# Kernel tuning notes

Hardware: AMD Instinct MI355X
Metric: run time of the kernel (lower is better)

## Reference

```python
import jax, jax.numpy as jnp
import numpy as np

B, S, D = 2, 2048, 2048
HQ, HK, HD = 16, 8, 128          # query heads, kv heads, head_dim
EPS = 1e-6
ROPE_THETA = 10000.0
SCALE = HD ** -0.5


def setup_inputs() -> dict:
    key = jax.random.key(0)
    ks = jax.random.split(key, 6)
    s = lambda fan_in: 1.0 / np.sqrt(fan_in)
    return {
        "hidden_states": jax.random.normal(ks[0], (B, S, D), jnp.float32),
        "positions": jnp.arange(S, dtype=jnp.int32),
        "Wq": jax.random.normal(ks[1], (D, HQ * HD), jnp.float32) * s(D),
        "Wk": jax.random.normal(ks[2], (D, HK * HD), jnp.float32) * s(D),
        "Wv": jax.random.normal(ks[3], (D, HK * HD), jnp.float32) * s(D),
        "Wo": jax.random.normal(ks[4], (HQ * HD, D), jnp.float32) * s(HQ * HD),
        "q_norm_w": jnp.ones((HD,), jnp.float32),
        "k_norm_w": jnp.ones((HD,), jnp.float32),
    }


def _rmsnorm(x, w):
    # RMSNorm over last (head_dim) axis, as in q_norm/k_norm
    var = jnp.mean(jnp.square(x), axis=-1, keepdims=True)
    return x * jax.lax.rsqrt(var + EPS) * w


def _rope(x, positions):
    # x: [B, S, H, HD]; rotate_half-style RoPE (Qwen3 convention)
    half = HD // 2
    inv_freq = 1.0 / (ROPE_THETA ** (jnp.arange(0, half, dtype=jnp.float32) / half))
    angles = positions.astype(jnp.float32)[:, None] * inv_freq[None, :]  # [S, half]
    cos = jnp.cos(angles)[None, :, None, :]  # [1, S, 1, half]
    sin = jnp.sin(angles)[None, :, None, :]
    x1, x2 = x[..., :half], x[..., half:]
    return jnp.concatenate([x1 * cos - x2 * sin, x2 * cos + x1 * sin], axis=-1)


def reference(hidden_states, positions, Wq, Wk, Wv, Wo, q_norm_w, k_norm_w):
    b, s, _ = hidden_states.shape
    q = (hidden_states @ Wq).reshape(b, s, HQ, HD)
    k = (hidden_states @ Wk).reshape(b, s, HK, HD)
    v = (hidden_states @ Wv).reshape(b, s, HK, HD)

    q = _rmsnorm(q, q_norm_w)
    k = _rmsnorm(k, k_norm_w)

    q = _rope(q, positions)
    k = _rope(k, positions)

    # GQA: repeat KV heads to match query heads
    groups = HQ // HK
    k = jnp.repeat(k, groups, axis=2)  # [B, S, HQ, HD]
    v = jnp.repeat(v, groups, axis=2)

    scores = jnp.einsum("bqhd,bkhd->bhqk", q, k) * SCALE  # [B, HQ, S, S]
    causal = jnp.tril(jnp.ones((s, s), dtype=bool))
    scores = jnp.where(causal[None, None], scores, jnp.float32(-jnp.inf))
    attn = jax.nn.softmax(scores, axis=-1)

    out = jnp.einsum("bhqk,bkhd->bqhd", attn, v).reshape(b, s, HQ * HD)
    return out @ Wo
```

## Files before the change

### kernel.cpp

```cpp
#include <hip/hip_runtime.h>
#include <cstdint>
#include <cstddef>

typedef _Float16 half8 __attribute__((ext_vector_type(8)));
typedef _Float16 half4 __attribute__((ext_vector_type(4)));
typedef float f32x4 __attribute__((ext_vector_type(4)));

#define DI __device__ __forceinline__

DI void gld_lds16(void* sp, const void* gp) {
  __builtin_amdgcn_global_load_lds(
      (const __attribute__((address_space(1))) void*)gp,
      (__attribute__((address_space(3))) void*)sp, 16, 0, 0);
}

template <int N>
DI void vmwait() { asm volatile("s_waitcnt vmcnt(%0)" :: "n"(N) : "memory"); }

DI void barrier_raw() {
  asm volatile("" ::: "memory");
  __builtin_amdgcn_s_barrier();
  asm volatile("" ::: "memory");
}

DI unsigned pk16(float a, float b) {
  _Float16 ha = (_Float16)a, hb = (_Float16)b;
  unsigned short ua = __builtin_bit_cast(unsigned short, ha);
  unsigned short ub = __builtin_bit_cast(unsigned short, hb);
  return (unsigned)ua | ((unsigned)ub << 16);
}

__global__ __launch_bounds__(256) void prep(const float* __restrict__ hs,
                                            const float* __restrict__ Wq,
                                            const float* __restrict__ Wk,
                                            const float* __restrict__ Wv,
                                            const float* __restrict__ Wo,
                                            _Float16* __restrict__ Xh,
                                            _Float16* __restrict__ Wqkvt,
                                            _Float16* __restrict__ Wot) {
  const int bid = blockIdx.x;
  if (bid >= 12288) {
    const int i = (bid - 12288) * 256 + threadIdx.x;
    const float4* p = (const float4*)hs + (size_t)i * 2;
    const float4 a = p[0], b = p[1];
    half8 h;
    h[0] = (_Float16)a.x; h[1] = (_Float16)a.y; h[2] = (_Float16)a.z; h[3] = (_Float16)a.w;
    h[4] = (_Float16)b.x; h[5] = (_Float16)b.y; h[6] = (_Float16)b.z; h[7] = (_Float16)b.w;
    *(half8*)(Xh + (size_t)i * 8) = h;
    return;
  }
  const float* in;
  _Float16* outp;
  int C, t;
  if (bid < 4096)      { in = Wq; outp = Wqkvt;                        C = 2048; t = bid; }
  else if (bid < 6144) { in = Wk; outp = Wqkvt + (size_t)2048 * 2048;  C = 1024; t = bid - 4096; }
  else if (bid < 8192) { in = Wv; outp = Wqkvt + (size_t)3072 * 2048;  C = 1024; t = bid - 6144; }
  else                 { in = Wo; outp = Wot;                          C = 2048; t = bid - 8192; }
  __shared__ float tl[32][33];
  const int tx = threadIdx.x & 31, ty = threadIdx.x >> 5;
  const int ctiles = C >> 5;
  const int tc = t % ctiles, tr = t / ctiles;
  const int r0 = tr * 32, c0 = tc * 32;
#pragma unroll
  for (int i = 0; i < 4; i++)
    tl[ty + 8 * i][tx] = in[(size_t)(r0 + ty + 8 * i) * C + c0 + tx];
  __syncthreads();
#pragma unroll
  for (int i = 0; i < 4; i++) {
    const int rr = ty + 8 * i;
    outp[(size_t)(c0 + rr) * 2048 + r0 + tx] = (_Float16)tl[tx][rr];
  }
}

#define QPHASE(Q, STAGE, VMW)                                                  \
  {                                                                            \
    half8 afr[2][2];                                                           \
    _Pragma("unroll") for (int j = 0; j < 2; j++)                              \
      _Pragma("unroll") for (int ks = 0; ks < 2; ks++) {                       \
        const int arow = wm * 128 + ((Q) * 2 + j) * 16 + lo;                   \
        afr[j][ks] =                                                           \
            *(const half8*)&sA[sa][arow * 64 + (((ks * 4 + hi) ^ lo7) << 3)];  \
      }                                                                        \
    STAGE;                                                                     \
    VMW;                                                                       \
    barrier_raw();                                                             \
    asm volatile("s_waitcnt lgkmcnt(0)" ::: "memory");                         \
    __builtin_amdgcn_sched_barrier(0);                                         \
    __builtin_amdgcn_s_setprio(1);                                             \
    _Pragma("unroll") for (int j = 0; j < 2; j++)                              \
      _Pragma("unroll") for (int nf = 0; nf < 4; nf++)                         \
        _Pragma("unroll") for (int ks = 0; ks < 2; ks++)                       \
          acc[(Q) * 2 + j][nf] = __builtin_amdgcn_mfma_f32_16x16x32_f16(       \
              afr[j][ks], bfr[nf][ks], acc[(Q) * 2 + j][nf], 0, 0, 0);         \
    __builtin_amdgcn_s_setprio(0);                                             \
    barrier_raw();                                                             \
  }

__global__ __launch_bounds__(512, 2) void gemm256(const _Float16* __restrict__ A,
                                                  const _Float16* __restrict__ Bt,
                                                  _Float16* __restrict__ C,
                                                  int M, int N, int K) {
  __shared__ _Float16 sA[3][16384];
  __shared__ _Float16 sB[2][16384];
  const int tid = threadIdx.x, w = tid >> 6, l = tid & 63, lo = l & 15, hi = l >> 4;
  const int lo7 = lo & 7;
  const int wm = w >> 2, wn = w & 3;
  const int nbn = N >> 8;
  const int nwg = gridDim.x;
  int bid = blockIdx.x;
  bid = (bid & 7) * (nwg >> 3) + (bid >> 3);
  const int bm0 = (bid / nbn) << 8, bn0 = (bid % nbn) << 8;
  const int cswz = ((tid & 7) ^ ((tid >> 3) & 7)) << 3;
  const int NT = K >> 6;

  auto stageA = [&](int kt, int slot, int i0) {
#pragma unroll
    for (int ii = 0; ii < 2; ++ii) {
      const int i = i0 + ii;
      gld_lds16(&sA[slot][i * 4096 + (w << 9)],
                A + (size_t)(bm0 + i * 64 + (tid >> 3)) * K + kt * 64 + cswz);
    }
  };
  auto stageB = [&](int kt, int slot, int i0) {
#pragma unroll
    for (int ii = 0; ii < 2; ++ii) {
      const int i = i0 + ii;
      gld_lds16(&sB[slot][i * 4096 + (w << 9)],
                Bt + (size_t)(bn0 + i * 64 + (tid >> 3)) * K + kt * 64 + cswz);
    }
  };

  f32x4 acc[8][4];
#pragma unroll
  for (int mf = 0; mf < 8; mf++)
#pragma unroll
    for (int nf = 0; nf < 4; nf++)
#pragma unroll
      for (int r = 0; r < 4; r++) acc[mf][nf][r] = 0.0f;

  stageA(0, 0, 0); stageA(0, 0, 2);
  stageA(1, 1, 0); stageA(1, 1, 2);
  stageB(0, 0, 0); stageB(0, 0, 2);
  vmwait<0>();
  barrier_raw();

  int sa = 0, sa2 = 2;
#pragma unroll 1
  for (int t = 0; t < NT; ++t) {
    const int sb = t & 1, sb1 = sb ^ 1;
    half8 bfr[4][2];
#pragma unroll
    for (int nf = 0; nf < 4; nf++)
#pragma unroll
      for (int ks = 0; ks < 2; ks++) {
        const int brow = wn * 64 + nf * 16 + lo;
        bfr[nf][ks] = *(const half8*)&sB[sb][brow * 64 + (((ks * 4 + hi) ^ lo7) << 3)];
      }
    QPHASE(0, if (t + 1 < NT) stageB(t + 1, sb1, 0), )
    QPHASE(1, if (t + 1 < NT) stageB(t + 1, sb1, 2), )
    QPHASE(2, if (t + 2 < NT) stageA(t + 2, sa2, 0), )
    QPHASE(3, if (t + 2 < NT) stageA(t + 2, sa2, 2),
           if (t + 2 < NT) { vmwait<4>(); } else { vmwait<0>(); })
    sa = (sa == 2) ? 0 : sa + 1;
    sa2 = (sa2 == 2) ? 0 : sa2 + 1;
  }

  const int nfsel = lo >> 2;
  const int sbase = hi * 16 + 4 * (lo & 3);
#pragma unroll
  for (int mf = 0; mf < 8; mf++)
#pragma unroll
    for (int r = 0; r < 4; r++) {
      const unsigned p01 = pk16(acc[mf][0][r], acc[mf][1][r]);
      const unsigned p23 = pk16(acc[mf][2][r], acc[mf][3][r]);
      unsigned h[4];
#pragma unroll
      for (int j = 0; j < 4; j++) {
        const unsigned w01 = (unsigned)__shfl((int)p01, sbase + j, 64);
        const unsigned w23 = (unsigned)__shfl((int)p23, sbase + j, 64);
        const unsigned wp = (nfsel & 2) ? w23 : w01;
        h[j] = (nfsel & 1) ? (wp >> 16) : (wp & 0xffffu);
      }
      const uint2 ov = make_uint2(h[0] | (h[1] << 16), h[2] | (h[3] << 16));
      *(uint2*)&C[(size_t)(bm0 + wm * 128 + mf * 16 + hi * 4 + r) * N +
                  (bn0 + wn * 64 + 4 * lo)] = ov;
    }
}

template <int BM, bool F16OUT>
__global__ __launch_bounds__(256) void gemm_bt(const _Float16* __restrict__ A,
                                               const _Float16* __restrict__ Bt,
                                               void* __restrict__ Cv,
                                               int M, int N, int K) {
  constexpr int MF = BM / 32;
  constexpr int LA = BM / 64;
  __shared__ _Float16 sA[2][BM * 32];
  __shared__ _Float16 sB[2][128 * 32];
  const int tid = threadIdx.x;
  const int w = tid >> 6, l = tid & 63, lo = l & 15, hi = l >> 4;
  const int gx = gridDim.x, nwg = gx * gridDim.y;
  int bid = blockIdx.y * gx + blockIdx.x;
  bid = (bid & 7) * (nwg >> 3) + (bid >> 3);
  const int bn0 = (bid % gx) * 128, bm0 = (bid / gx) * BM;
  const int wm = w >> 1, wn = w & 1;
  const int srow = l >> 2;
  const int csel = ((l & 3) ^ ((l >> 3) & 3)) * 8;
  const int kswz = (hi ^ ((lo >> 1) & 3)) * 8;

  f32x4 acc[MF][4];
#pragma unroll
  for (int mi = 0; mi < MF; mi++)
#pragma unroll
    for (int ni = 0; ni < 4; ni++)
#pragma unroll
      for (int r = 0; r < 4; r++) acc[mi][ni][r] = 0.0f;

  auto stage = [&](int bi, int kt) {
#pragma unroll
    for (int i = 0; i < LA; ++i) {
      const int j = LA * w + i;
      gld_lds16(&sA[bi][j * 512],
                A + (size_t)(bm0 + j * 16 + srow) * K + (size_t)kt * 32 + csel);
    }
#pragma unroll
    for (int i = 0; i < 2; ++i) {
      const int j = 2 * w + i;
      gld_lds16(&sB[bi][j * 512],
                Bt + (size_t)(bn0 + j * 16 + srow) * K + (size_t)kt * 32 + csel);
    }
  };

  stage(0, 0);
  __syncthreads();
  const int KT = K >> 5;
#pragma unroll 1
  for (int kt = 0; kt < KT; ++kt) {
    const int cur = kt & 1;
    if (kt + 1 < KT) stage(cur ^ 1, kt + 1);
    half8 a[MF], b[4];
#pragma unroll
    for (int mi = 0; mi < MF; mi++)
      a[mi] = *(const half8*)&sA[cur][(wm * (BM / 2) + mi * 16 + lo) * 32 + kswz];
#pragma unroll
    for (int ni = 0; ni < 4; ni++)
      b[ni] = *(const half8*)&sB[cur][(wn * 64 + ni * 16 + lo) * 32 + kswz];
#pragma unroll
    for (int mi = 0; mi < MF; mi++)
#pragma unroll
      for (int ni = 0; ni < 4; ni++)
        acc[mi][ni] = __builtin_amdgcn_mfma_f32_16x16x32_f16(a[mi], b[ni], acc[mi][ni], 0, 0, 0);
    __syncthreads();
  }

#pragma unroll
  for (int mi = 0; mi < MF; mi++)
#pragma unroll
    for (int ni = 0; ni < 4; ni++)
#pragma unroll
      for (int r = 0; r < 4; r++) {
        const size_t idx = (size_t)(bm0 + wm * (BM / 2) + mi * 16 + hi * 4 + r) * N +
                           (bn0 + wn * 64 + ni * 16 + lo);
        if constexpr (F16OUT) ((_Float16*)Cv)[idx] = (_Float16)acc[mi][ni][r];
        else                  ((float*)Cv)[idx] = acc[mi][ni][r];
      }
}

__global__ __launch_bounds__(256) void post(const _Float16* __restrict__ QKV,
                                            const int* __restrict__ pos,
                                            const float* __restrict__ qw,
                                            const float* __restrict__ kw,
                                            _Float16* __restrict__ Qb,
                                            _Float16* __restrict__ Kb,
                                            _Float16* __restrict__ Vt) {
  if (blockIdx.x >= 24576) {
    __shared__ _Float16 tt[32][34];
    const int g = blockIdx.x - 24576;
    const int tx = threadIdx.x & 31, ty = threadIdx.x >> 5;
    const int dt = g & 3;
    const int st = (g >> 2) & 63;
    const int bh = g >> 8;
    const _Float16* src = QKV + (size_t)((bh >> 3) * 2048 + st * 32) * 4096 +
                          3072 + (bh & 7) * 128 + dt * 32;
#pragma unroll
    for (int i = 0; i < 4; i++)
      tt[ty + 8 * i][tx] = src[(size_t)(ty + 8 * i) * 4096 + tx];
    __syncthreads();
    _Float16* dst = Vt + ((size_t)bh * 128 + dt * 32) * 2048 + st * 32;
#pragma unroll
    for (int i = 0; i < 4; i++) {
      const int rr = ty + 8 * i;
      dst[(size_t)rr * 2048 + tx] = tt[tx][rr];
    }
    return;
  }
  const int w = threadIdx.x >> 6, l = threadIdx.x & 63;
  const int wv = blockIdx.x * 4 + w;
  const int t = wv / 24, hh = wv - t * 24;
  const int b = t >> 11, s = t & 2047;
  const bool isq = hh < 16;
  const int col = isq ? hh * 128 : 2048 + (hh - 16) * 128;
  const _Float16* x = QKV + (size_t)t * 4096 + col;
  const float x1 = (float)x[l], x2 = (float)x[l + 64];
  float ss = x1 * x1 + x2 * x2;
  ss += __shfl_xor(ss, 32); ss += __shfl_xor(ss, 16); ss += __shfl_xor(ss, 8);
  ss += __shfl_xor(ss, 4);  ss += __shfl_xor(ss, 2);  ss += __shfl_xor(ss, 1);
  const float rn = rsqrtf(ss * 0.0078125f + 1e-6f);
  const float* wt = isq ? qw : kw;
  const float n1 = x1 * rn * wt[l], n2 = x2 * rn * wt[l + 64];
  const float ang = (float)pos[s] * exp2f((float)l * -0.2076205059304601f);
  float sa, ca;
  sincosf(ang, &sa, &ca);
  const float qs = isq ? 0.12751731f : 1.0f;
  const float o1 = (n1 * ca - n2 * sa) * qs;
  const float o2 = (n2 * ca + n1 * sa) * qs;
  _Float16* dst = isq ? Qb + (((size_t)b * 16 + hh) * 2048 + s) * 128
                      : Kb + (((size_t)b * 8 + (hh - 16)) * 2048 + s) * 128;
  dst[l] = (_Float16)o1;
  dst[l + 64] = (_Float16)o2;
}

__global__ __launch_bounds__(256) void attn_fwd(const _Float16* __restrict__ Q,
                                                const _Float16* __restrict__ K,
                                                const _Float16* __restrict__ Vt,
                                                _Float16* __restrict__ AO) {
  __shared__ _Float16 sK[2][64 * 128];
  __shared__ _Float16 sV[2][128 * 64];
  __shared__ _Float16 P[4][16 * 72];
  const int tid = threadIdx.x, w = tid >> 6, l = tid & 63, lo = l & 15, hi = l >> 4;
  const int qt = 31 - (blockIdx.x >> 5);
  const int hq = blockIdx.x & 15;
  const int b = (blockIdx.x >> 4) & 1;
  const int hk = hq >> 1, q0 = qt * 64;
  const _Float16* Qh = Q + ((size_t)(b * 16 + hq) * 2048) * 128;
  const _Float16* Kh = K + ((size_t)(b * 8 + hk) * 2048) * 128;
  const _Float16* Vh = Vt + ((size_t)(b * 8 + hk) * 128) * 2048;
  const int qw0 = q0 + w * 16;

  auto stageK = [&](int bi, int kv0) {
#pragma unroll
    for (int i = 0; i < 4; ++i) {
      const int inst = w * 4 + i;
      const int r = inst * 4 + (l >> 4);
      const int cb = ((l & 15) * 16) ^ ((r & 7) << 4);
      gld_lds16(&sK[bi][inst * 512],
                (const char*)Kh + (size_t)(kv0 + r) * 256 + cb);
    }
  };
  auto stageV = [&](int bi, int kv0) {
#pragma unroll
    for (int i = 0; i < 4; ++i) {
      const int inst = w * 4 + i;
      const int r = inst * 8 + (l >> 3);
      const int cb = ((l & 7) * 16) ^ ((r & 7) << 4);
      gld_lds16(&sV[bi][inst * 512],
                (const char*)Vh + (size_t)r * 4096 + (size_t)kv0 * 2 + cb);
    }
  };

  half8 aq[4];
#pragma unroll
  for (int kc = 0; kc < 4; kc++)
    aq[kc] = *(const half8*)(Qh + (size_t)(qw0 + lo) * 128 + kc * 32 + hi * 8);

  f32x4 o[8];
#pragma unroll
  for (int dn = 0; dn < 8; dn++)
#pragma unroll
    for (int r = 0; r < 4; r++) o[dn][r] = 0.0f;
  float mrow = -1e30f, lrow = 0.0f;

  const int nt = qt + 1;
  stageK(0, 0);
  stageV(0, 0);
  __syncthreads();
#pragma unroll 1
  for (int kt = 0; kt < nt; ++kt) {
    const int kv0 = kt * 64;
    const int cur = kt & 1;
    if (kt + 1 < nt) {
      stageK(cur ^ 1, kv0 + 64);
      stageV(cur ^ 1, kv0 + 64);
    }
    const char* kb = (const char*)sK[cur];
    const char* vb = (const char*)sV[cur];
    f32x4 s[4];
#pragma unroll
    for (int ns = 0; ns < 4; ns++) {
#pragma unroll
      for (int r = 0; r < 4; r++) s[ns][r] = 0.0f;
      const int krow = ns * 16 + lo;
#pragma unroll
      for (int kc = 0; kc < 4; kc++) {
        half8 bk = *(const half8*)(kb + krow * 256 +
                                   ((kc * 64 + hi * 16) ^ ((krow & 7) << 4)));
        s[ns] = __builtin_amdgcn_mfma_f32_16x16x32_f16(bk, aq[kc], s[ns], 0, 0, 0);
      }
    }
    if (kt == nt - 1) {
#pragma unroll
      for (int ns = 0; ns < 4; ns++) {
        const int kv = kv0 + ns * 16 + hi * 4;
#pragma unroll
        for (int r = 0; r < 4; r++)
          if (kv + r > qw0 + lo) s[ns][r] = -1e30f;
      }
    }
    float tmax = s[0][0];
#pragma unroll
    for (int ns = 0; ns < 4; ns++)
#pragma unroll
      for (int r = 0; r < 4; r++) tmax = fmaxf(tmax, s[ns][r]);
    tmax = fmaxf(tmax, __shfl_xor(tmax, 16));
    tmax = fmaxf(tmax, __shfl_xor(tmax, 32));
    if (!__all(tmax <= mrow + 8.0f)) {
      const float mn = fmaxf(mrow, tmax);
      const float corr = exp2f(mrow - mn);
      mrow = mn;
      lrow *= corr;
      float c4[4];
#pragma unroll
      for (int r = 0; r < 4; r++) c4[r] = __shfl(corr, hi * 4 + r, 16);
#pragma unroll
      for (int dn = 0; dn < 8; dn++)
#pragma unroll
        for (int r = 0; r < 4; r++) o[dn][r] *= c4[r];
    }
    float psum = 0.0f;
#pragma unroll
    for (int ns = 0; ns < 4; ns++) {
      half4 pk;
#pragma unroll
      for (int r = 0; r < 4; r++) {
        const float p = exp2f(s[ns][r] - mrow);
        psum += p;
        pk[r] = (_Float16)p;
      }
      *(half4*)&P[w][lo * 72 + ns * 16 + hi * 4] = pk;
    }
    psum += __shfl_xor(psum, 16);
    psum += __shfl_xor(psum, 32);
    lrow += psum;
    asm volatile("s_waitcnt lgkmcnt(0)" ::: "memory");
    half8 ap0 = *(const half8*)&P[w][lo * 72 + hi * 8];
    half8 ap1 = *(const half8*)&P[w][lo * 72 + 32 + hi * 8];
#pragma unroll
    for (int dn = 0; dn < 8; dn++) {
      const int vrow = dn * 16 + lo;
      half8 bv0 = *(const half8*)(vb + vrow * 128 + ((hi * 16) ^ ((vrow & 7) << 4)));
      half8 bv1 = *(const half8*)(vb + vrow * 128 + ((64 + hi * 16) ^ ((vrow & 7) << 4)));
      o[dn] = __builtin_amdgcn_mfma_f32_16x16x32_f16(ap0, bv0, o[dn], 0, 0, 0);
      o[dn] = __builtin_amdgcn_mfma_f32_16x16x32_f16(ap1, bv1, o[dn], 0, 0, 0);
    }
    __syncthreads();
  }

  const float inv = 1.0f / lrow;
  float i4[4];
#pragma unroll
  for (int r = 0; r < 4; r++) i4[r] = __shfl(inv, hi * 4 + r, 16);
  const size_t tok = (size_t)b * 2048 + qw0;
#pragma unroll
  for (int dn = 0; dn < 8; dn++)
#pragma unroll
    for (int r = 0; r < 4; r++)
      AO[(tok + hi * 4 + r) * 2048 + hq * 128 + dn * 16 + lo] = (_Float16)(o[dn][r] * i4[r]);
}

extern "C" void kernel_launch(void* const* d_in, const int* in_sizes, int n_in,
                              void* d_out, int out_size, void* d_ws, size_t ws_size,
                              hipStream_t stream) {
  (void)in_sizes; (void)n_in; (void)out_size; (void)ws_size;
  const float* hs  = (const float*)d_in[0];
  const int*   pos = (const int*)d_in[1];
  const float* Wq  = (const float*)d_in[2];
  const float* Wk  = (const float*)d_in[3];
  const float* Wv  = (const float*)d_in[4];
  const float* Wo  = (const float*)d_in[5];
  const float* qnw = (const float*)d_in[6];
  const float* knw = (const float*)d_in[7];
  float* out = (float*)d_out;

  char* ws = (char*)d_ws;
  size_t off = 0;
  auto take = [&](size_t bytes) -> void* {
    void* p = ws + off;
    off += (bytes + 255) & ~(size_t)255;
    return p;
  };
  _Float16* Xh    = (_Float16*)take((size_t)4096 * 2048 * 2);
  _Float16* Wqkvt = (_Float16*)take((size_t)4096 * 2048 * 2);
  _Float16* Wot   = (_Float16*)take((size_t)2048 * 2048 * 2);
  _Float16* QKVh  = (_Float16*)take((size_t)4096 * 4096 * 2);
  _Float16* Qb    = (_Float16*)take((size_t)2 * 16 * 2048 * 128 * 2);
  _Float16* Kb    = (_Float16*)take((size_t)2 * 8 * 2048 * 128 * 2);
  _Float16* Vt    = (_Float16*)take((size_t)2 * 8 * 128 * 2048 * 2);
  _Float16* AO    = (_Float16*)take((size_t)4096 * 2048 * 2);

  prep<<<16384, 256, 0, stream>>>(hs, Wq, Wk, Wv, Wo, Xh, Wqkvt, Wot);
  gemm256<<<256, 512, 0, stream>>>(Xh, Wqkvt, QKVh, 4096, 4096, 2048);
  post<<<28672, 256, 0, stream>>>(QKVh, pos, qnw, knw, Qb, Kb, Vt);
  attn_fwd<<<1024, 256, 0, stream>>>(Qb, Kb, Vt, AO);
  gemm_bt<64, false><<<dim3(16, 64), 256, 0, stream>>>(AO, Wot, out, 4096, 2048, 2048);
}
```

Before: 233.1 us.

## Enlarge attention query tile to 128 rows with two 16-row groups per warp

The attention kernel now handles 128 query rows per block, with each warp processing two 16-row groups that share every K/V tile staged into LDS. This halves the K/V global-to-LDS traffic per query and halves the grid to 512 blocks. Tiles are scheduled in a pairing order (15-qi for the first 8 groups, then ascending) to balance the causal workload. In exchange, register pressure roughly doubles (two accumulator sets and two Q fragments), which may lower occupancy, and fewer blocks means less parallelism across CUs.

```diff
diff --git a/kernel.cpp b/kernel.cpp
--- a/kernel.cpp
+++ b/kernel.cpp
@@ -327,14 +327,15 @@
   __shared__ _Float16 sV[2][128 * 64];
   __shared__ _Float16 P[4][16 * 72];
   const int tid = threadIdx.x, w = tid >> 6, l = tid & 63, lo = l & 15, hi = l >> 4;
-  const int qt = 31 - (blockIdx.x >> 5);
+  const int qi = blockIdx.x >> 5;
+  const int qt = (qi < 8) ? (15 - qi) : (qi - 8);
   const int hq = blockIdx.x & 15;
   const int b = (blockIdx.x >> 4) & 1;
-  const int hk = hq >> 1, q0 = qt * 64;
+  const int hk = hq >> 1, q0 = qt * 128;
   const _Float16* Qh = Q + ((size_t)(b * 16 + hq) * 2048) * 128;
   const _Float16* Kh = K + ((size_t)(b * 8 + hk) * 2048) * 128;
   const _Float16* Vh = Vt + ((size_t)(b * 8 + hk) * 128) * 2048;
-  const int qw0 = q0 + w * 16;
+  const int qw0 = q0 + w * 32;
 
   auto stageK = [&](int bi, int kv0) {
 #pragma unroll
@@ -357,19 +358,23 @@
     }
   };
 
-  half8 aq[4];
-#pragma unroll
-  for (int kc = 0; kc < 4; kc++)
-    aq[kc] = *(const half8*)(Qh + (size_t)(qw0 + lo) * 128 + kc * 32 + hi * 8);
-
-  f32x4 o[8];
-#pragma unroll
-  for (int dn = 0; dn < 8; dn++)
-#pragma unroll
-    for (int r = 0; r < 4; r++) o[dn][r] = 0.0f;
-  float mrow = -1e30f, lrow = 0.0f;
-
-  const int nt = qt + 1;
+  half8 aq[2][4];
+#pragma unroll
+  for (int g = 0; g < 2; g++)
+#pragma unroll
+    for (int kc = 0; kc < 4; kc++)
+      aq[g][kc] = *(const half8*)(Qh + (size_t)(qw0 + g * 16 + lo) * 128 + kc * 32 + hi * 8);
+
+  f32x4 o[2][8];
+#pragma unroll
+  for (int g = 0; g < 2; g++)
+#pragma unroll
+    for (int dn = 0; dn < 8; dn++)
+#pragma unroll
+      for (int r = 0; r < 4; r++) o[g][dn][r] = 0.0f;
+  float mrow[2] = {-1e30f, -1e30f}, lrow[2] = {0.0f, 0.0f};
+
+  const int nt = (qt + 1) * 2;
   stageK(0, 0);
   stageV(0, 0);
   __syncthreads();
@@ -383,87 +388,97 @@
     }
     const char* kb = (const char*)sK[cur];
     const char* vb = (const char*)sV[cur];
-    f32x4 s[4];
+    f32x4 s[2][4];
 #pragma unroll
     for (int ns = 0; ns < 4; ns++) {
 #pragma unroll
-      for (int r = 0; r < 4; r++) s[ns][r] = 0.0f;
+      for (int r = 0; r < 4; r++) { s[0][ns][r] = 0.0f; s[1][ns][r] = 0.0f; }
       const int krow = ns * 16 + lo;
 #pragma unroll
       for (int kc = 0; kc < 4; kc++) {
         half8 bk = *(const half8*)(kb + krow * 256 +
                                    ((kc * 64 + hi * 16) ^ ((krow & 7) << 4)));
-        s[ns] = __builtin_amdgcn_mfma_f32_16x16x32_f16(bk, aq[kc], s[ns], 0, 0, 0);
-      }
-    }
-    if (kt == nt - 1) {
+        s[0][ns] = __builtin_amdgcn_mfma_f32_16x16x32_f16(bk, aq[0][kc], s[0][ns], 0, 0, 0);
+        s[1][ns] = __builtin_amdgcn_mfma_f32_16x16x32_f16(bk, aq[1][kc], s[1][ns], 0, 0, 0);
+      }
+    }
+    if (kt >= nt - 2) {
+#pragma unroll
+      for (int g = 0; g < 2; g++)
+#pragma unroll
+        for (int ns = 0; ns < 4; ns++) {
+          const int kv = kv0 + ns * 16 + hi * 4;
+#pragma unroll
+          for (int r = 0; r < 4; r++)
+            if (kv + r > qw0 + g * 16 + lo) s[g][ns][r] = -1e30f;
+        }
+    }
+#pragma unroll
+    for (int g = 0; g < 2; g++) {
+      float tmax = s[g][0][0];
+#pragma unroll
+      for (int ns = 0; ns < 4; ns++)
+#pragma unroll
+        for (int r = 0; r < 4; r++) tmax = fmaxf(tmax, s[g][ns][r]);
+      tmax = fmaxf(tmax, __shfl_xor(tmax, 16));
+      tmax = fmaxf(tmax, __shfl_xor(tmax, 32));
+      if (!__all(tmax <= mrow[g] + 8.0f)) {
+        const float mn = fmaxf(mrow[g], tmax);
+        const float corr = exp2f(mrow[g] - mn);
+        mrow[g] = mn;
+        lrow[g] *= corr;
+        float c4[4];
+#pragma unroll
+        for (int r = 0; r < 4; r++) c4[r] = __shfl(corr, hi * 4 + r, 16);
+#pragma unroll
+        for (int dn = 0; dn < 8; dn++)
+#pragma unroll
+          for (int r = 0; r < 4; r++) o[g][dn][r] *= c4[r];
+      }
+      float psum = 0.0f;
 #pragma unroll
       for (int ns = 0; ns < 4; ns++) {
-        const int kv = kv0 + ns * 16 + hi * 4;
-#pragma unroll
-        for (int r = 0; r < 4; r++)
-          if (kv + r > qw0 + lo) s[ns][r] = -1e30f;
-      }
-    }
-    float tmax = s[0][0];
-#pragma unroll
-    for (int ns = 0; ns < 4; ns++)
-#pragma unroll
-      for (int r = 0; r < 4; r++) tmax = fmaxf(tmax, s[ns][r]);
-    tmax = fmaxf(tmax, __shfl_xor(tmax, 16));
-    tmax = fmaxf(tmax, __shfl_xor(tmax, 32));
-    if (!__all(tmax <= mrow + 8.0f)) {
-      const float mn = fmaxf(mrow, tmax);
-      const float corr = exp2f(mrow - mn);
-      mrow = mn;
-      lrow *= corr;
-      float c4[4];
-#pragma unroll
-      for (int r = 0; r < 4; r++) c4[r] = __shfl(corr, hi * 4 + r, 16);
-#pragma unroll
-      for (int dn = 0; dn < 8; dn++)
-#pragma unroll
-        for (int r = 0; r < 4; r++) o[dn][r] *= c4[r];
-    }
-    float psum = 0.0f;
-#pragma unroll
-    for (int ns = 0; ns < 4; ns++) {
-      half4 pk;
-#pragma unroll
-      for (int r = 0; r < 4; r++) {
-        const float p = exp2f(s[ns][r] - mrow);
-        psum += p;
-        pk[r] = (_Float16)p;
-      }
-      *(half4*)&P[w][lo * 72 + ns * 16 + hi * 4] = pk;
-    }
-    psum += __shfl_xor(psum, 16);
-    psum += __shfl_xor(psum, 32);
-    lrow += psum;
-    asm volatile("s_waitcnt lgkmcnt(0)" ::: "memory");
-    half8 ap0 = *(const half8*)&P[w][lo * 72 + hi * 8];
-    half8 ap1 = *(const half8*)&P[w][lo * 72 + 32 + hi * 8];
-#pragma unroll
-    for (int dn = 0; dn < 8; dn++) {
-      const int vrow = dn * 16 + lo;
-      half8 bv0 = *(const half8*)(vb + vrow * 128 + ((hi * 16) ^ ((vrow & 7) << 4)));
-      half8 bv1 = *(const half8*)(vb + vrow * 128 + ((64 + hi * 16) ^ ((vrow & 7) << 4)));
-      o[dn] = __builtin_amdgcn_mfma_f32_16x16x32_f16(ap0, bv0, o[dn], 0, 0, 0);
-      o[dn] = __builtin_amdgcn_mfma_f32_16x16x32_f16(ap1, bv1, o[dn], 0, 0, 0);
+        half4 pk;
+#pragma unroll
+        for (int r = 0; r < 4; r++) {
+          const float p = exp2f(s[g][ns][r] - mrow[g]);
+          psum += p;
+          pk[r] = (_Float16)p;
+        }
+        *(half4*)&P[w][lo * 72 + ns * 16 + hi * 4] = pk;
+      }
+      psum += __shfl_xor(psum, 16);
+      psum += __shfl_xor(psum, 32);
+      lrow[g] += psum;
+      asm volatile("s_waitcnt lgkmcnt(0)" ::: "memory");
+      half8 ap0 = *(const half8*)&P[w][lo * 72 + hi * 8];
+      half8 ap1 = *(const half8*)&P[w][lo * 72 + 32 + hi * 8];
+#pragma unroll
+      for (int dn = 0; dn < 8; dn++) {
+        const int vrow = dn * 16 + lo;
+        half8 bv0 = *(const half8*)(vb + vrow * 128 + ((hi * 16) ^ ((vrow & 7) << 4)));
+        half8 bv1 = *(const half8*)(vb + vrow * 128 + ((64 + hi * 16) ^ ((vrow & 7) << 4)));
+        o[g][dn] = __builtin_amdgcn_mfma_f32_16x16x32_f16(ap0, bv0, o[g][dn], 0, 0, 0);
+        o[g][dn] = __builtin_amdgcn_mfma_f32_16x16x32_f16(ap1, bv1, o[g][dn], 0, 0, 0);
+      }
     }
     __syncthreads();
   }
 
-  const float inv = 1.0f / lrow;
-  float i4[4];
-#pragma unroll
-  for (int r = 0; r < 4; r++) i4[r] = __shfl(inv, hi * 4 + r, 16);
   const size_t tok = (size_t)b * 2048 + qw0;
 #pragma unroll
-  for (int dn = 0; dn < 8; dn++)
-#pragma unroll
-    for (int r = 0; r < 4; r++)
-      AO[(tok + hi * 4 + r) * 2048 + hq * 128 + dn * 16 + lo] = (_Float16)(o[dn][r] * i4[r]);
+  for (int g = 0; g < 2; g++) {
+    const float inv = 1.0f / lrow[g];
+    float i4[4];
+#pragma unroll
+    for (int r = 0; r < 4; r++) i4[r] = __shfl(inv, hi * 4 + r, 16);
+#pragma unroll
+    for (int dn = 0; dn < 8; dn++)
+#pragma unroll
+      for (int r = 0; r < 4; r++)
+        AO[(tok + g * 16 + hi * 4 + r) * 2048 + hq * 128 + dn * 16 + lo] =
+            (_Float16)(o[g][dn][r] * i4[r]);
+  }
 }
 
 extern "C" void kernel_launch(void* const* d_in, const int* in_sizes, int n_in,
@@ -499,6 +514,6 @@
   prep<<<16384, 256, 0, stream>>>(hs, Wq, Wk, Wv, Wo, Xh, Wqkvt, Wot);
   gemm256<<<256, 512, 0, stream>>>(Xh, Wqkvt, QKVh, 4096, 4096, 2048);
   post<<<28672, 256, 0, stream>>>(QKVh, pos, qnw, knw, Qb, Kb, Vt);
-  attn_fwd<<<1024, 256, 0, stream>>>(Qb, Kb, Vt, AO);
+  attn_fwd<<<512, 256, 0, stream>>>(Qb, Kb, Vt, AO);
   gemm_bt<64, false><<<dim3(16, 64), 256, 0, stream>>>(AO, Wot, out, 4096, 2048, 2048);
 }
```

New measurement: 276.1 us. 1.18x slower.
